# Performance work log

Measured on AMD Instinct MI355X. Metric: run time of the kernel, lower is better.

The kernel has to match this reference:

```python
import jax, jax.numpy as jnp
import numpy as np

N_NODES = 100000
N_EDGES = 1600000
F_IN, F_HID, F_OUT = 128, 256, 128


def setup_inputs() -> dict:
    key = jax.random.key(0)
    ks = jax.random.split(key, 9)
    x = jax.random.normal(ks[0], (N_NODES, F_IN), dtype=jnp.float32)
    edge_src = jax.random.randint(ks[1], (N_EDGES,), 0, N_NODES, dtype=jnp.int32)
    edge_dst = jax.random.randint(ks[2], (N_EDGES,), 0, N_NODES, dtype=jnp.int32)
    s1 = 1.0 / np.sqrt(F_IN)
    s2 = 1.0 / np.sqrt(F_HID)
    W_self1 = jax.random.uniform(ks[3], (F_IN, F_HID), jnp.float32, -s1, s1)
    W_neigh1 = jax.random.uniform(ks[4], (F_IN, F_HID), jnp.float32, -s1, s1)
    b1 = jnp.zeros((F_HID,), jnp.float32)
    W_self2 = jax.random.uniform(ks[5], (F_HID, F_OUT), jnp.float32, -s2, s2)
    W_neigh2 = jax.random.uniform(ks[6], (F_HID, F_OUT), jnp.float32, -s2, s2)
    b2 = jnp.zeros((F_OUT,), jnp.float32)
    return {"x": x, "edge_src": edge_src, "edge_dst": edge_dst,
            "W_self1": W_self1, "W_neigh1": W_neigh1, "b1": b1,
            "W_self2": W_self2, "W_neigh2": W_neigh2, "b2": b2}


def _sage_mean(h, src, dst, W_self, W_neigh, b):
    # mean-aggregate neighbor features onto dst nodes (DGL SAGEConv 'mean')
    deg = jax.ops.segment_sum(jnp.ones_like(src, dtype=h.dtype), dst,
                              num_segments=N_NODES)
    neigh_sum = jax.ops.segment_sum(h[src], dst, num_segments=N_NODES)
    neigh = neigh_sum / jnp.maximum(deg, 1.0)[:, None]
    return h @ W_self + neigh @ W_neigh + b


def reference(x, edge_src, edge_dst, W_self1, W_neigh1, b1, W_self2, W_neigh2, b2):
    h = _sage_mean(x, edge_src, edge_dst, W_self1, W_neigh1, b1)
    h = jax.nn.sigmoid(h)
    h = _sage_mean(h, edge_src, edge_dst, W_self2, W_neigh2, b2)
    return h
```

## Files before the change

### kernel.cpp

```cpp
#include <hip/hip_runtime.h>
#include <hip/hip_bf16.h>

#define N_NODES 100000
#define N_EDGES 1600000
#define F_IN 128
#define F_HID 256
#define F_OUT 128

typedef unsigned short ushort_t;
typedef __attribute__((ext_vector_type(4))) float f32x4;
typedef __attribute__((ext_vector_type(8))) short bf16x8;

#define GAS __attribute__((address_space(1)))
#define LAS __attribute__((address_space(3)))

__device__ __forceinline__ float bf2f(ushort_t u) {
    unsigned int x = ((unsigned int)u) << 16;
    return __builtin_bit_cast(float, x);
}
__device__ __forceinline__ ushort_t f2bf(float f) {
    unsigned int x = __builtin_bit_cast(unsigned int, f);
    unsigned int r = (x + 0x7fffu + ((x >> 16) & 1u)) >> 16;
    return (ushort_t)r;
}

#define NBUCK ((N_NODES + 255) >> 8)
#define CHUNK 4096

__global__ __launch_bounds__(256) void bucket_count_kernel(
    const int* __restrict__ dst, int* __restrict__ bucket_cnt, int n) {
    __shared__ int hist[NBUCK];
    int tid = threadIdx.x;
    int e0 = blockIdx.x * CHUNK;
    int cnt = n - e0; if (cnt > CHUNK) cnt = CHUNK;
    for (int b = tid; b < NBUCK; b += 256) hist[b] = 0;
    __syncthreads();
    for (int i = tid; i < cnt; i += 256) {
        int d = __builtin_nontemporal_load(dst + e0 + i);
        atomicAdd(&hist[d >> 8], 1);
    }
    __syncthreads();
    for (int b = tid; b < NBUCK; b += 256)
        if (hist[b]) atomicAdd(&bucket_cnt[b], hist[b]);
}

__global__ __launch_bounds__(512) void bucket_scan_kernel(
    const int* __restrict__ bucket_cnt, int* __restrict__ bbase,
    int* __restrict__ bcursor, int* __restrict__ rowptr) {
    __shared__ int tmp[512];
    int tid = threadIdx.x;
    int v = (tid < NBUCK) ? bucket_cnt[tid] : 0;
    tmp[tid] = v;
    __syncthreads();
#pragma unroll
    for (int off = 1; off < 512; off <<= 1) {
        int t = (tid >= off) ? tmp[tid - off] : 0;
        __syncthreads();
        tmp[tid] += t;
        __syncthreads();
    }
    if (tid < NBUCK) {
        int base = tmp[tid] - v;
        bbase[tid] = base;
        bcursor[tid] = base;
    }
    if (tid == 0) {
        bbase[NBUCK] = N_EDGES;
        rowptr[N_NODES] = N_EDGES;
    }
}

__global__ __launch_bounds__(256) void bin_edges_kernel(
    const int* __restrict__ src, const int* __restrict__ dst,
    int* __restrict__ bcursor, unsigned int* __restrict__ pairs, int n) {
    __shared__ int sdst[CHUNK];
    __shared__ int ssrc[CHUNK];
    __shared__ int hist[NBUCK];
    __shared__ int resv[NBUCK];
    int tid = threadIdx.x;
    int e0 = blockIdx.x * CHUNK;
    int cnt = n - e0; if (cnt > CHUNK) cnt = CHUNK;
    for (int b = tid; b < NBUCK; b += 256) hist[b] = 0;
    __syncthreads();
    for (int i = tid; i < cnt; i += 256) {
        int d = __builtin_nontemporal_load(dst + e0 + i);
        int s = __builtin_nontemporal_load(src + e0 + i);
        sdst[i] = d;
        ssrc[i] = s;
        atomicAdd(&hist[d >> 8], 1);
    }
    __syncthreads();
    for (int b = tid; b < NBUCK; b += 256) {
        int h = hist[b];
        resv[b] = h ? atomicAdd(&bcursor[b], h) : 0;
        hist[b] = 0;
    }
    __syncthreads();
    for (int i = tid; i < cnt; i += 256) {
        int d = sdst[i], s = ssrc[i];
        int b = d >> 8;
        int off = atomicAdd(&hist[b], 1);
        pairs[resv[b] + off] = ((unsigned)(d & 255) << 17) | (unsigned)s;
    }
}

__global__ __launch_bounds__(256) void sort_bucket_kernel(
    const unsigned int* __restrict__ pairs, const int* __restrict__ bbase,
    int* __restrict__ rowptr, float* __restrict__ invdeg,
    int* __restrict__ csr_src, int nNodes) {
    __shared__ int lcnt[256];
    __shared__ int lrp[256];
    int tid = threadIdx.x;
    int base = blockIdx.x << 8;
    int nn = nNodes - base; if (nn > 256) nn = 256;
    lcnt[tid] = 0;
    __syncthreads();
    int e0 = bbase[blockIdx.x], e1 = bbase[blockIdx.x + 1];
    for (int i = e0 + tid; i < e1; i += 256)
        atomicAdd(&lcnt[pairs[i] >> 17], 1);
    __syncthreads();
    int v = lcnt[tid];
    lrp[tid] = v;
    __syncthreads();
#pragma unroll
    for (int off = 1; off < 256; off <<= 1) {
        int t = (tid >= off) ? lrp[tid - off] : 0;
        __syncthreads();
        lrp[tid] += t;
        __syncthreads();
    }
    lcnt[tid] = 0;
    lrp[tid] = lrp[tid] - v + e0;
    if (tid < nn) {
        rowptr[base + tid] = lrp[tid];
        invdeg[base + tid] = 1.0f / fmaxf((float)v, 1.0f);
    }
    __syncthreads();
    for (int i = e0 + tid; i < e1; i += 256) {
        unsigned pv = pairs[i];
        int j = (int)(pv >> 17);
        int off = atomicAdd(&lcnt[j], 1);
        csr_src[lrp[j] + off] = (int)(pv & 0x1FFFFu);
    }
}

__global__ __launch_bounds__(256) void convert_x_kernel(const float* __restrict__ x,
                                                        ushort_t* __restrict__ xb, int n4) {
    int i = blockIdx.x * 256 + threadIdx.x;
    if (i >= n4) return;
    int e = i * 4;
    f32x4 v = __builtin_nontemporal_load((const f32x4*)(x + e));
    ushort4 o;
    o.x = f2bf(v.x); o.y = f2bf(v.y); o.z = f2bf(v.z); o.w = f2bf(v.w);
    *(ushort4*)(xb + e) = o;
}

__global__ __launch_bounds__(256) void wtransK_kernel(const float* __restrict__ W1,
                                                      const float* __restrict__ W2,
                                                      ushort_t* __restrict__ Wt,
                                                      int Kx, int Ktot, int N) {
    int i = blockIdx.x * 256 + threadIdx.x;
    if (i >= N * Ktot) return;
    int n = i / Ktot, k = i - n * Ktot;
    float v = (k < Kx) ? W1[(size_t)k * N + n] : W2[(size_t)(k - Kx) * N + n];
    Wt[(size_t)n * Ktot + k] = f2bf(v);
}

__global__ __launch_bounds__(256) void wtransN_kernel(const float* __restrict__ Wa,
                                                      const float* __restrict__ Wb,
                                                      ushort_t* __restrict__ Wt,
                                                      int K, int Nh) {
    int i = blockIdx.x * 256 + threadIdx.x;
    if (i >= 2 * Nh * K) return;
    int n = i / K, k = i - n * K;
    const float* W = (n < Nh) ? Wa : Wb;
    int nn = (n < Nh) ? n : n - Nh;
    Wt[(size_t)n * K + k] = f2bf(W[(size_t)k * Nh + nn]);
}

#define ACC8(arr, v)                                                \
    arr[0] += bf2f((ushort_t)((v).x & 0xffffu));                    \
    arr[1] += bf2f((ushort_t)((v).x >> 16));                        \
    arr[2] += bf2f((ushort_t)((v).y & 0xffffu));                    \
    arr[3] += bf2f((ushort_t)((v).y >> 16));                        \
    arr[4] += bf2f((ushort_t)((v).z & 0xffffu));                    \
    arr[5] += bf2f((ushort_t)((v).z >> 16));                        \
    arr[6] += bf2f((ushort_t)((v).w & 0xffffu));                    \
    arr[7] += bf2f((ushort_t)((v).w >> 16));

template <int MODE>
__global__ __launch_bounds__(256) void gather2_kernel(
    const ushort_t* __restrict__ H,
    const int* __restrict__ rowptr,
    const int* __restrict__ csr_src,
    const float* __restrict__ invdeg,
    const ushort_t* __restrict__ uself,
    const float* __restrict__ bias,
    void* __restrict__ outp,
    int nNodes, int totWaves) {
    int lane = threadIdx.x & 63;
    int wv = blockIdx.x * 4 + (threadIdx.x >> 6);
    int grp = lane >> 4, sub = lane & 15;
    const size_t cofs = (size_t)sub * 8;
    int pair = wv;
    if (pair * 2 >= nNodes) return;
    int r0 = rowptr[pair * 2];
    int r1 = rowptr[pair * 2 + 1];
    int r2 = rowptr[pair * 2 + 2];
    while (true) {
        int npair = pair + totWaves;
        bool hasNext = (npair * 2 < nNodes);
        int n0 = 0, n1 = 0, n2 = 0;
        if (hasNext) {
            n0 = rowptr[npair * 2];
            n1 = rowptr[npair * 2 + 1];
            n2 = rowptr[npair * 2 + 2];
        }
        int nodeA = pair * 2;
        int sA = r0, eA = r1, sB = r1, eB = r2;
        int cA = sA < N_EDGES ? sA : N_EDGES - 1;
        int cB = sB < N_EDGES ? sB : N_EDGES - 1;
        float accA[8] = {}, accB[8] = {};
        for (int ea = sA + grp, eb = sB + grp; ea < eA || eb < eB; ea += 16, eb += 16) {
            bool pa0 = ea < eA, pa1 = ea + 4 < eA, pa2 = ea + 8 < eA, pa3 = ea + 12 < eA;
            bool pb0 = eb < eB, pb1 = eb + 4 < eB, pb2 = eb + 8 < eB, pb3 = eb + 12 < eB;
            int ja0 = pa0 ? ea : cA, ja1 = pa1 ? ea + 4 : cA;
            int ja2 = pa2 ? ea + 8 : cA, ja3 = pa3 ? ea + 12 : cA;
            int jb0 = pb0 ? eb : cB, jb1 = pb1 ? eb + 4 : cB;
            int jb2 = pb2 ? eb + 8 : cB, jb3 = pb3 ? eb + 12 : cB;
            int sa0 = csr_src[ja0], sa1 = csr_src[ja1];
            int sa2 = csr_src[ja2], sa3 = csr_src[ja3];
            int sb0 = csr_src[jb0], sb1 = csr_src[jb1];
            int sb2 = csr_src[jb2], sb3 = csr_src[jb3];
            uint4 va0 = *(const uint4*)(H + (size_t)sa0 * 128 + cofs);
            uint4 va1 = *(const uint4*)(H + (size_t)sa1 * 128 + cofs);
            uint4 va2 = *(const uint4*)(H + (size_t)sa2 * 128 + cofs);
            uint4 va3 = *(const uint4*)(H + (size_t)sa3 * 128 + cofs);
            uint4 vb0 = *(const uint4*)(H + (size_t)sb0 * 128 + cofs);
            uint4 vb1 = *(const uint4*)(H + (size_t)sb1 * 128 + cofs);
            uint4 vb2 = *(const uint4*)(H + (size_t)sb2 * 128 + cofs);
            uint4 vb3 = *(const uint4*)(H + (size_t)sb3 * 128 + cofs);
            if (pa0) { ACC8(accA, va0); }
            if (pa1) { ACC8(accA, va1); }
            if (pa2) { ACC8(accA, va2); }
            if (pa3) { ACC8(accA, va3); }
            if (pb0) { ACC8(accB, vb0); }
            if (pb1) { ACC8(accB, vb1); }
            if (pb2) { ACC8(accB, vb2); }
            if (pb3) { ACC8(accB, vb3); }
        }
#pragma unroll
        for (int j = 0; j < 8; ++j) {
            accA[j] += __shfl_xor(accA[j], 16);
            accA[j] += __shfl_xor(accA[j], 32);
            accB[j] += __shfl_xor(accB[j], 16);
            accB[j] += __shfl_xor(accB[j], 32);
        }
        if (grp == 0) {
            int nodeB = nodeA + 1;
            float scA = invdeg[nodeA];
            float scB = (nodeB < nNodes) ? invdeg[nodeB] : 1.0f;
            if (MODE == 0) {
                uint4 o;
                o.x = (unsigned)f2bf(accA[0] * scA) | ((unsigned)f2bf(accA[1] * scA) << 16);
                o.y = (unsigned)f2bf(accA[2] * scA) | ((unsigned)f2bf(accA[3] * scA) << 16);
                o.z = (unsigned)f2bf(accA[4] * scA) | ((unsigned)f2bf(accA[5] * scA) << 16);
                o.w = (unsigned)f2bf(accA[6] * scA) | ((unsigned)f2bf(accA[7] * scA) << 16);
                *(uint4*)((ushort_t*)outp + (size_t)nodeA * 128 + cofs) = o;
                if (nodeB < nNodes) {
                    uint4 p2;
                    p2.x = (unsigned)f2bf(accB[0] * scB) | ((unsigned)f2bf(accB[1] * scB) << 16);
                    p2.y = (unsigned)f2bf(accB[2] * scB) | ((unsigned)f2bf(accB[3] * scB) << 16);
                    p2.z = (unsigned)f2bf(accB[4] * scB) | ((unsigned)f2bf(accB[5] * scB) << 16);
                    p2.w = (unsigned)f2bf(accB[6] * scB) | ((unsigned)f2bf(accB[7] * scB) << 16);
                    *(uint4*)((ushort_t*)outp + (size_t)nodeB * 128 + cofs) = p2;
                }
            } else {
                uint4 us = *(const uint4*)(uself + (size_t)nodeA * 128 + cofs);
                f32x4 o0, o1;
                o0.x = accA[0] * scA + bf2f((ushort_t)(us.x & 0xffffu)) + bias[cofs + 0];
                o0.y = accA[1] * scA + bf2f((ushort_t)(us.x >> 16)) + bias[cofs + 1];
                o0.z = accA[2] * scA + bf2f((ushort_t)(us.y & 0xffffu)) + bias[cofs + 2];
                o0.w = accA[3] * scA + bf2f((ushort_t)(us.y >> 16)) + bias[cofs + 3];
                o1.x = accA[4] * scA + bf2f((ushort_t)(us.z & 0xffffu)) + bias[cofs + 4];
                o1.y = accA[5] * scA + bf2f((ushort_t)(us.z >> 16)) + bias[cofs + 5];
                o1.z = accA[6] * scA + bf2f((ushort_t)(us.w & 0xffffu)) + bias[cofs + 6];
                o1.w = accA[7] * scA + bf2f((ushort_t)(us.w >> 16)) + bias[cofs + 7];
                float* op = (float*)outp + (size_t)nodeA * 128 + cofs;
                __builtin_nontemporal_store(o0, (f32x4*)op);
                __builtin_nontemporal_store(o1, (f32x4*)(op + 4));
                if (nodeB < nNodes) {
                    uint4 u2 = *(const uint4*)(uself + (size_t)nodeB * 128 + cofs);
                    f32x4 q0, q1;
                    q0.x = accB[0] * scB + bf2f((ushort_t)(u2.x & 0xffffu)) + bias[cofs + 0];
                    q0.y = accB[1] * scB + bf2f((ushort_t)(u2.x >> 16)) + bias[cofs + 1];
                    q0.z = accB[2] * scB + bf2f((ushort_t)(u2.y & 0xffffu)) + bias[cofs + 2];
                    q0.w = accB[3] * scB + bf2f((ushort_t)(u2.y >> 16)) + bias[cofs + 3];
                    q1.x = accB[4] * scB + bf2f((ushort_t)(u2.z & 0xffffu)) + bias[cofs + 4];
                    q1.y = accB[5] * scB + bf2f((ushort_t)(u2.z >> 16)) + bias[cofs + 5];
                    q1.z = accB[6] * scB + bf2f((ushort_t)(u2.w & 0xffffu)) + bias[cofs + 6];
                    q1.w = accB[7] * scB + bf2f((ushort_t)(u2.w >> 16)) + bias[cofs + 7];
                    float* oq = (float*)outp + (size_t)nodeB * 128 + cofs;
                    __builtin_nontemporal_store(q0, (f32x4*)oq);
                    __builtin_nontemporal_store(q1, (f32x4*)(oq + 4));
                }
            }
        }
        if (!hasNext) break;
        pair = npair; r0 = n0; r1 = n1; r2 = n2;
    }
}

__global__ __launch_bounds__(512) void gemm_fused_kernel(
    const ushort_t* __restrict__ xb,
    const ushort_t* __restrict__ agg,
    const ushort_t* __restrict__ Wt1,
    const float* __restrict__ b1,
    const ushort_t* __restrict__ Wt2,
    ushort_t* __restrict__ uself,
    ushort_t* __restrict__ uneigh,
    int M) {
    __shared__ ushort_t hs[64 * 256];
    __shared__ ushort_t Asb[2][64 * 32];
    __shared__ ushort_t Bsb[2][256 * 32];
    int tid = threadIdx.x;
    int lane = tid & 63, wid = tid >> 6;
    int l15 = lane & 15, kgrp = lane >> 4;
    int bm = blockIdx.x * 64;
    int wr = (wid >> 2) * 32, wc = (wid & 3) * 64;

    auto stageA = [&](int buf, int t) {
        if (wid >= 4) return;
        int k0 = t * 32;
        const ushort_t* Ap = (k0 < 128) ? xb : agg;
        int kk0 = k0 & 127;
        int row = wid * 16 + (lane >> 2);
        int scol = ((lane & 3) ^ (row & 3)) << 3;
        int ar = bm + row; if (ar > M - 1) ar = M - 1;
        __builtin_amdgcn_global_load_lds(
            (const GAS void*)(Ap + (size_t)ar * 128 + kk0 + scol),
            (LAS void*)(&Asb[buf][wid * 512]), 16, 0, 0);
    };
    auto stageB = [&](int buf, int t, const ushort_t* Bt) {
        int k0 = t * 32;
#pragma unroll
        for (int t2 = 0; t2 < 2; ++t2) {
            int c = wid * 2 + t2;
            int row = c * 16 + (lane >> 2);
            int scol = ((lane & 3) ^ (row & 3)) << 3;
            __builtin_amdgcn_global_load_lds(
                (const GAS void*)(Bt + (size_t)row * 256 + k0 + scol),
                (LAS void*)(&Bsb[buf][c * 512]), 16, 0, 0);
        }
    };

    f32x4 acc[2][4] = {};

    stageA(0, 0); stageB(0, 0, Wt1);
    __syncthreads();
#pragma unroll
    for (int t = 0; t < 8; ++t) {
        int buf = t & 1;
        if (t < 7) { stageA(buf ^ 1, t + 1); stageB(buf ^ 1, t + 1, Wt1); }
        bf16x8 af[2], bfv[4];
#pragma unroll
        for (int mi = 0; mi < 2; ++mi) {
            int row = wr + mi * 16 + l15;
            af[mi] = *(const bf16x8*)(&Asb[buf][row * 32 + ((kgrp ^ (row & 3)) << 3)]);
        }
#pragma unroll
        for (int ni = 0; ni < 4; ++ni) {
            int row = wc + ni * 16 + l15;
            bfv[ni] = *(const bf16x8*)(&Bsb[buf][row * 32 + ((kgrp ^ (row & 3)) << 3)]);
        }
#pragma unroll
        for (int mi = 0; mi < 2; ++mi)
#pragma unroll
            for (int ni = 0; ni < 4; ++ni)
                acc[mi][ni] = __builtin_amdgcn_mfma_f32_16x16x32_bf16(
                    af[mi], bfv[ni], acc[mi][ni], 0, 0, 0);
        __syncthreads();
    }

#pragma unroll
    for (int mi = 0; mi < 2; ++mi) {
#pragma unroll
        for (int ni = 0; ni < 4; ++ni) {
            int hcol = wc + ni * 16 + l15;
            float bv = b1[hcol];
#pragma unroll
            for (int r = 0; r < 4; ++r) {
                float v = acc[mi][ni][r] + bv;
                v = 1.0f / (1.0f + __expf(-v));
                int lr = wr + mi * 16 + kgrp * 4 + r;
                hs[lr * 256 + (hcol ^ ((lr & 7) << 3))] = f2bf(v);
                acc[mi][ni][r] = 0.0f;
            }
        }
    }
    stageB(0, 0, Wt2);
    __syncthreads();
#pragma unroll
    for (int t = 0; t < 8; ++t) {
        int buf = t & 1;
        if (t < 7) stageB(buf ^ 1, t + 1, Wt2);
        int k0 = t * 32;
        bf16x8 af[2], bfv[4];
#pragma unroll
        for (int mi = 0; mi < 2; ++mi) {
            int row = wr + mi * 16 + l15;
            int c = k0 + kgrp * 8;
            af[mi] = *(const bf16x8*)(&hs[row * 256 + (c ^ ((row & 7) << 3))]);
        }
#pragma unroll
        for (int ni = 0; ni < 4; ++ni) {
            int row = wc + ni * 16 + l15;
            bfv[ni] = *(const bf16x8*)(&Bsb[buf][row * 32 + ((kgrp ^ (row & 3)) << 3)]);
        }
#pragma unroll
        for (int mi = 0; mi < 2; ++mi)
#pragma unroll
            for (int ni = 0; ni < 4; ++ni)
                acc[mi][ni] = __builtin_amdgcn_mfma_f32_16x16x32_bf16(
                    af[mi], bfv[ni], acc[mi][ni], 0, 0, 0);
        __syncthreads();
    }

    ushort_t* my = hs + wid * 1024;
#pragma unroll
    for (int mi = 0; mi < 2; ++mi) {
#pragma unroll
        for (int ni = 0; ni < 4; ++ni) {
#pragma unroll
            for (int r = 0; r < 4; ++r) {
                int lr = kgrp * 4 + r;
                int lc = (ni * 16 + l15) ^ (kgrp << 3);
                my[lr * 64 + lc] = f2bf(acc[mi][ni][r]);
            }
        }
#pragma unroll
        for (int it = 0; it < 2; ++it) {
            int r2 = (lane >> 3) + it * 8;
            int swz = ((r2 >> 2) & 3) << 3;
            int c2 = ((lane & 7) << 3) ^ swz;
            bf16x8 vv = *(const bf16x8*)(&my[r2 * 64 + c2]);
            int grow = bm + wr + mi * 16 + r2;
            if (grow < M) {
                int gc = wc + (c2 ^ swz);
                ushort_t* dstp = (gc < 128)
                    ? uself + (size_t)grow * 128 + gc
                    : uneigh + (size_t)grow * 128 + (gc - 128);
                *(bf16x8*)dstp = vv;
            }
        }
    }
}

extern "C" void kernel_launch(void* const* d_in, const int* in_sizes, int n_in,
                              void* d_out, int out_size, void* d_ws, size_t ws_size,
                              hipStream_t stream) {
    const float* x        = (const float*)d_in[0];
    const int*   src      = (const int*)d_in[1];
    const int*   dst      = (const int*)d_in[2];
    const float* W_self1  = (const float*)d_in[3];
    const float* W_neigh1 = (const float*)d_in[4];
    const float* b1       = (const float*)d_in[5];
    const float* W_self2  = (const float*)d_in[6];
    const float* W_neigh2 = (const float*)d_in[7];
    const float* b2       = (const float*)d_in[8];
    float* out = (float*)d_out;

    char* p = (char*)d_ws;
    auto alloc = [&](size_t bytes) { char* r = p; p += (bytes + 255) & ~(size_t)255; return r; };
    float*    invdeg   = (float*)alloc((size_t)N_NODES * 4);
    ushort_t* xb       = (ushort_t*)alloc((size_t)N_NODES * 128 * 2);
    ushort_t* agg      = (ushort_t*)alloc((size_t)N_NODES * 128 * 2);
    ushort_t* uself    = (ushort_t*)alloc((size_t)N_NODES * 128 * 2);
    ushort_t* uneigh   = (ushort_t*)alloc((size_t)N_NODES * 128 * 2);
    ushort_t* Wt1      = (ushort_t*)alloc((size_t)256 * 256 * 2);
    ushort_t* Wt2      = (ushort_t*)alloc((size_t)256 * 256 * 2);
    int* rowptr        = (int*)alloc((size_t)(N_NODES + 1) * 4);
    int* bucket_cnt    = (int*)alloc((size_t)NBUCK * 4);
    int* bbase         = (int*)alloc((size_t)(NBUCK + 1) * 4);
    int* bcursor       = (int*)alloc((size_t)NBUCK * 4);
    unsigned int* pairs= (unsigned int*)alloc((size_t)N_EDGES * 4);
    int* csr_src       = (int*)alloc((size_t)N_EDGES * 4);

    convert_x_kernel<<<(N_NODES * F_IN / 4 + 255) / 256, 256, 0, stream>>>(
        x, xb, N_NODES * F_IN / 4);
    wtransK_kernel<<<(256 * 256 + 255) / 256, 256, 0, stream>>>(
        W_self1, W_neigh1, Wt1, 128, 256, 256);
    wtransN_kernel<<<(256 * 256 + 255) / 256, 256, 0, stream>>>(
        W_self2, W_neigh2, Wt2, 256, 128);

    hipMemsetAsync(bucket_cnt, 0, (size_t)NBUCK * sizeof(int), stream);
    bucket_count_kernel<<<(N_EDGES + CHUNK - 1) / CHUNK, 256, 0, stream>>>(
        dst, bucket_cnt, N_EDGES);
    bucket_scan_kernel<<<1, 512, 0, stream>>>(bucket_cnt, bbase, bcursor, rowptr);
    bin_edges_kernel<<<(N_EDGES + CHUNK - 1) / CHUNK, 256, 0, stream>>>(
        src, dst, bcursor, pairs, N_EDGES);
    sort_bucket_kernel<<<NBUCK, 256, 0, stream>>>(
        pairs, bbase, rowptr, invdeg, csr_src, N_NODES);

    const int GATHER_BLOCKS = 2048;
    const int TOT_WAVES = GATHER_BLOCKS * 4;

    gather2_kernel<0><<<GATHER_BLOCKS, 256, 0, stream>>>(
        xb, rowptr, csr_src, invdeg, nullptr, nullptr, agg, N_NODES, TOT_WAVES);
    {
        dim3 grid((N_NODES + 63) / 64);
        gemm_fused_kernel<<<grid, 512, 0, stream>>>(
            xb, agg, Wt1, b1, Wt2, uself, uneigh, N_NODES);
    }
    gather2_kernel<1><<<GATHER_BLOCKS, 256, 0, stream>>>(
        uneigh, rowptr, csr_src, invdeg, uself, b2, out, N_NODES, TOT_WAVES);
}
```

Baseline: 273.5 us.

## Replace count/scan binning with fixed-capacity buckets and fuse weight transposes

Drops the bucket-count and bucket-scan kernels by giving each destination bucket a fixed capacity region (BCAP slots), so bin_edges can scatter directly using per-bucket cursors. Row boundaries become start/end int2 pairs per node, since the CSR is no longer contiguous. The two weight-transpose kernels are merged into one launch. This removes launches and a full pass over dst, but relies on no bucket exceeding 8192 edges and enlarges the pairs and csr_src buffers.

```diff
diff --git a/kernel.cpp b/kernel.cpp
--- a/kernel.cpp
+++ b/kernel.cpp
@@ -26,49 +26,7 @@
 
 #define NBUCK ((N_NODES + 255) >> 8)
 #define CHUNK 4096
-
-__global__ __launch_bounds__(256) void bucket_count_kernel(
-    const int* __restrict__ dst, int* __restrict__ bucket_cnt, int n) {
-    __shared__ int hist[NBUCK];
-    int tid = threadIdx.x;
-    int e0 = blockIdx.x * CHUNK;
-    int cnt = n - e0; if (cnt > CHUNK) cnt = CHUNK;
-    for (int b = tid; b < NBUCK; b += 256) hist[b] = 0;
-    __syncthreads();
-    for (int i = tid; i < cnt; i += 256) {
-        int d = __builtin_nontemporal_load(dst + e0 + i);
-        atomicAdd(&hist[d >> 8], 1);
-    }
-    __syncthreads();
-    for (int b = tid; b < NBUCK; b += 256)
-        if (hist[b]) atomicAdd(&bucket_cnt[b], hist[b]);
-}
-
-__global__ __launch_bounds__(512) void bucket_scan_kernel(
-    const int* __restrict__ bucket_cnt, int* __restrict__ bbase,
-    int* __restrict__ bcursor, int* __restrict__ rowptr) {
-    __shared__ int tmp[512];
-    int tid = threadIdx.x;
-    int v = (tid < NBUCK) ? bucket_cnt[tid] : 0;
-    tmp[tid] = v;
-    __syncthreads();
-#pragma unroll
-    for (int off = 1; off < 512; off <<= 1) {
-        int t = (tid >= off) ? tmp[tid - off] : 0;
-        __syncthreads();
-        tmp[tid] += t;
-        __syncthreads();
-    }
-    if (tid < NBUCK) {
-        int base = tmp[tid] - v;
-        bbase[tid] = base;
-        bcursor[tid] = base;
-    }
-    if (tid == 0) {
-        bbase[NBUCK] = N_EDGES;
-        rowptr[N_NODES] = N_EDGES;
-    }
-}
+#define BCAP 8192
 
 __global__ __launch_bounds__(256) void bin_edges_kernel(
     const int* __restrict__ src, const int* __restrict__ dst,
@@ -92,7 +50,7 @@
     __syncthreads();
     for (int b = tid; b < NBUCK; b += 256) {
         int h = hist[b];
-        resv[b] = h ? atomicAdd(&bcursor[b], h) : 0;
+        resv[b] = h ? (b * BCAP + atomicAdd(&bcursor[b], h)) : 0;
         hist[b] = 0;
     }
     __syncthreads();
@@ -105,8 +63,8 @@
 }
 
 __global__ __launch_bounds__(256) void sort_bucket_kernel(
-    const unsigned int* __restrict__ pairs, const int* __restrict__ bbase,
-    int* __restrict__ rowptr, float* __restrict__ invdeg,
+    const unsigned int* __restrict__ pairs, const int* __restrict__ bcursor,
+    int2* __restrict__ rowse, float* __restrict__ invdeg,
     int* __restrict__ csr_src, int nNodes) {
     __shared__ int lcnt[256];
     __shared__ int lrp[256];
@@ -115,7 +73,8 @@
     int nn = nNodes - base; if (nn > 256) nn = 256;
     lcnt[tid] = 0;
     __syncthreads();
-    int e0 = bbase[blockIdx.x], e1 = bbase[blockIdx.x + 1];
+    int e0 = blockIdx.x * BCAP;
+    int e1 = e0 + bcursor[blockIdx.x];
     for (int i = e0 + tid; i < e1; i += 256)
         atomicAdd(&lcnt[pairs[i] >> 17], 1);
     __syncthreads();
@@ -132,7 +91,7 @@
     lcnt[tid] = 0;
     lrp[tid] = lrp[tid] - v + e0;
     if (tid < nn) {
-        rowptr[base + tid] = lrp[tid];
+        rowse[base + tid] = make_int2(lrp[tid], lrp[tid] + v);
         invdeg[base + tid] = 1.0f / fmaxf((float)v, 1.0f);
     }
     __syncthreads();
@@ -155,27 +114,22 @@
     *(ushort4*)(xb + e) = o;
 }
 
-__global__ __launch_bounds__(256) void wtransK_kernel(const float* __restrict__ W1,
-                                                      const float* __restrict__ W2,
-                                                      ushort_t* __restrict__ Wt,
-                                                      int Kx, int Ktot, int N) {
+__global__ __launch_bounds__(256) void wtrans_both_kernel(
+    const float* __restrict__ Ws1, const float* __restrict__ Wn1,
+    const float* __restrict__ Ws2, const float* __restrict__ Wn2,
+    ushort_t* __restrict__ Wt1, ushort_t* __restrict__ Wt2) {
     int i = blockIdx.x * 256 + threadIdx.x;
-    if (i >= N * Ktot) return;
-    int n = i / Ktot, k = i - n * Ktot;
-    float v = (k < Kx) ? W1[(size_t)k * N + n] : W2[(size_t)(k - Kx) * N + n];
-    Wt[(size_t)n * Ktot + k] = f2bf(v);
-}
-
-__global__ __launch_bounds__(256) void wtransN_kernel(const float* __restrict__ Wa,
-                                                      const float* __restrict__ Wb,
-                                                      ushort_t* __restrict__ Wt,
-                                                      int K, int Nh) {
-    int i = blockIdx.x * 256 + threadIdx.x;
-    if (i >= 2 * Nh * K) return;
-    int n = i / K, k = i - n * K;
-    const float* W = (n < Nh) ? Wa : Wb;
-    int nn = (n < Nh) ? n : n - Nh;
-    Wt[(size_t)n * K + k] = f2bf(W[(size_t)k * Nh + nn]);
+    if (i < 65536) {
+        int n = i >> 8, k = i & 255;
+        float v = (k < 128) ? Ws1[(size_t)k * 256 + n] : Wn1[(size_t)(k - 128) * 256 + n];
+        Wt1[(size_t)n * 256 + k] = f2bf(v);
+    } else {
+        int j = i - 65536;
+        int n = j >> 8, k = j & 255;
+        const float* W = (n < 128) ? Ws2 : Wn2;
+        int nn = (n < 128) ? n : n - 128;
+        Wt2[(size_t)n * 256 + k] = f2bf(W[(size_t)k * 128 + nn]);
+    }
 }
 
 #define ACC8(arr, v)                                                \
@@ -191,7 +145,7 @@
 template <int MODE>
 __global__ __launch_bounds__(256) void gather2_kernel(
     const ushort_t* __restrict__ H,
-    const int* __restrict__ rowptr,
+    const int2* __restrict__ rowse,
     const int* __restrict__ csr_src,
     const float* __restrict__ invdeg,
     const ushort_t* __restrict__ uself,
@@ -204,22 +158,19 @@
     const size_t cofs = (size_t)sub * 8;
     int pair = wv;
     if (pair * 2 >= nNodes) return;
-    int r0 = rowptr[pair * 2];
-    int r1 = rowptr[pair * 2 + 1];
-    int r2 = rowptr[pair * 2 + 2];
+    int2 ra = rowse[pair * 2];
+    int2 rb = rowse[pair * 2 + 1];
     while (true) {
         int npair = pair + totWaves;
         bool hasNext = (npair * 2 < nNodes);
-        int n0 = 0, n1 = 0, n2 = 0;
+        int2 na = make_int2(0, 0), nb = make_int2(0, 0);
         if (hasNext) {
-            n0 = rowptr[npair * 2];
-            n1 = rowptr[npair * 2 + 1];
-            n2 = rowptr[npair * 2 + 2];
+            na = rowse[npair * 2];
+            nb = rowse[npair * 2 + 1];
         }
         int nodeA = pair * 2;
-        int sA = r0, eA = r1, sB = r1, eB = r2;
-        int cA = sA < N_EDGES ? sA : N_EDGES - 1;
-        int cB = sB < N_EDGES ? sB : N_EDGES - 1;
+        int sA = ra.x, eA = ra.y, sB = rb.x, eB = rb.y;
+        int cA = sA, cB = sB;
         float accA[8] = {}, accB[8] = {};
         for (int ea = sA + grp, eb = sB + grp; ea < eA || eb < eB; ea += 16, eb += 16) {
             bool pa0 = ea < eA, pa1 = ea + 4 < eA, pa2 = ea + 8 < eA, pa3 = ea + 12 < eA;
@@ -259,7 +210,7 @@
         if (grp == 0) {
             int nodeB = nodeA + 1;
             float scA = invdeg[nodeA];
-            float scB = (nodeB < nNodes) ? invdeg[nodeB] : 1.0f;
+            float scB = invdeg[nodeB];
             if (MODE == 0) {
                 uint4 o;
                 o.x = (unsigned)f2bf(accA[0] * scA) | ((unsigned)f2bf(accA[1] * scA) << 16);
@@ -267,14 +218,12 @@
                 o.z = (unsigned)f2bf(accA[4] * scA) | ((unsigned)f2bf(accA[5] * scA) << 16);
                 o.w = (unsigned)f2bf(accA[6] * scA) | ((unsigned)f2bf(accA[7] * scA) << 16);
                 *(uint4*)((ushort_t*)outp + (size_t)nodeA * 128 + cofs) = o;
-                if (nodeB < nNodes) {
-                    uint4 p2;
-                    p2.x = (unsigned)f2bf(accB[0] * scB) | ((unsigned)f2bf(accB[1] * scB) << 16);
-                    p2.y = (unsigned)f2bf(accB[2] * scB) | ((unsigned)f2bf(accB[3] * scB) << 16);
-                    p2.z = (unsigned)f2bf(accB[4] * scB) | ((unsigned)f2bf(accB[5] * scB) << 16);
-                    p2.w = (unsigned)f2bf(accB[6] * scB) | ((unsigned)f2bf(accB[7] * scB) << 16);
-                    *(uint4*)((ushort_t*)outp + (size_t)nodeB * 128 + cofs) = p2;
-                }
+                uint4 p2;
+                p2.x = (unsigned)f2bf(accB[0] * scB) | ((unsigned)f2bf(accB[1] * scB) << 16);
+                p2.y = (unsigned)f2bf(accB[2] * scB) | ((unsigned)f2bf(accB[3] * scB) << 16);
+                p2.z = (unsigned)f2bf(accB[4] * scB) | ((unsigned)f2bf(accB[5] * scB) << 16);
+                p2.w = (unsigned)f2bf(accB[6] * scB) | ((unsigned)f2bf(accB[7] * scB) << 16);
+                *(uint4*)((ushort_t*)outp + (size_t)nodeB * 128 + cofs) = p2;
             } else {
                 uint4 us = *(const uint4*)(uself + (size_t)nodeA * 128 + cofs);
                 f32x4 o0, o1;
@@ -289,25 +238,23 @@
                 float* op = (float*)outp + (size_t)nodeA * 128 + cofs;
                 __builtin_nontemporal_store(o0, (f32x4*)op);
                 __builtin_nontemporal_store(o1, (f32x4*)(op + 4));
-                if (nodeB < nNodes) {
-                    uint4 u2 = *(const uint4*)(uself + (size_t)nodeB * 128 + cofs);
-                    f32x4 q0, q1;
-                    q0.x = accB[0] * scB + bf2f((ushort_t)(u2.x & 0xffffu)) + bias[cofs + 0];
-                    q0.y = accB[1] * scB + bf2f((ushort_t)(u2.x >> 16)) + bias[cofs + 1];
-                    q0.z = accB[2] * scB + bf2f((ushort_t)(u2.y & 0xffffu)) + bias[cofs + 2];
-                    q0.w = accB[3] * scB + bf2f((ushort_t)(u2.y >> 16)) + bias[cofs + 3];
-                    q1.x = accB[4] * scB + bf2f((ushort_t)(u2.z & 0xffffu)) + bias[cofs + 4];
-                    q1.y = accB[5] * scB + bf2f((ushort_t)(u2.z >> 16)) + bias[cofs + 5];
-                    q1.z = accB[6] * scB + bf2f((ushort_t)(u2.w & 0xffffu)) + bias[cofs + 6];
-                    q1.w = accB[7] * scB + bf2f((ushort_t)(u2.w >> 16)) + bias[cofs + 7];
-                    float* oq = (float*)outp + (size_t)nodeB * 128 + cofs;
-                    __builtin_nontemporal_store(q0, (f32x4*)oq);
-                    __builtin_nontemporal_store(q1, (f32x4*)(oq + 4));
-                }
+                uint4 u2 = *(const uint4*)(uself + (size_t)nodeB * 128 + cofs);
+                f32x4 q0, q1;
+                q0.x = accB[0] * scB + bf2f((ushort_t)(u2.x & 0xffffu)) + bias[cofs + 0];
+                q0.y = accB[1] * scB + bf2f((ushort_t)(u2.x >> 16)) + bias[cofs + 1];
+                q0.z = accB[2] * scB + bf2f((ushort_t)(u2.y & 0xffffu)) + bias[cofs + 2];
+                q0.w = accB[3] * scB + bf2f((ushort_t)(u2.y >> 16)) + bias[cofs + 3];
+                q1.x = accB[4] * scB + bf2f((ushort_t)(u2.z & 0xffffu)) + bias[cofs + 4];
+                q1.y = accB[5] * scB + bf2f((ushort_t)(u2.z >> 16)) + bias[cofs + 5];
+                q1.z = accB[6] * scB + bf2f((ushort_t)(u2.w & 0xffffu)) + bias[cofs + 6];
+                q1.w = accB[7] * scB + bf2f((ushort_t)(u2.w >> 16)) + bias[cofs + 7];
+                float* oq = (float*)outp + (size_t)nodeB * 128 + cofs;
+                __builtin_nontemporal_store(q0, (f32x4*)oq);
+                __builtin_nontemporal_store(q1, (f32x4*)(oq + 4));
             }
         }
         if (!hasNext) break;
-        pair = npair; r0 = n0; r1 = n1; r2 = n2;
+        pair = npair; ra = na; rb = nb;
     }
 }
 
@@ -479,39 +426,32 @@
     ushort_t* uneigh   = (ushort_t*)alloc((size_t)N_NODES * 128 * 2);
     ushort_t* Wt1      = (ushort_t*)alloc((size_t)256 * 256 * 2);
     ushort_t* Wt2      = (ushort_t*)alloc((size_t)256 * 256 * 2);
-    int* rowptr        = (int*)alloc((size_t)(N_NODES + 1) * 4);
-    int* bucket_cnt    = (int*)alloc((size_t)NBUCK * 4);
-    int* bbase         = (int*)alloc((size_t)(NBUCK + 1) * 4);
+    int2* rowse        = (int2*)alloc((size_t)N_NODES * 8);
     int* bcursor       = (int*)alloc((size_t)NBUCK * 4);
-    unsigned int* pairs= (unsigned int*)alloc((size_t)N_EDGES * 4);
-    int* csr_src       = (int*)alloc((size_t)N_EDGES * 4);
+    unsigned int* pairs= (unsigned int*)alloc((size_t)NBUCK * BCAP * 4);
+    int* csr_src       = (int*)alloc((size_t)NBUCK * BCAP * 4);
 
     convert_x_kernel<<<(N_NODES * F_IN / 4 + 255) / 256, 256, 0, stream>>>(
         x, xb, N_NODES * F_IN / 4);
-    wtransK_kernel<<<(256 * 256 + 255) / 256, 256, 0, stream>>>(
-        W_self1, W_neigh1, Wt1, 128, 256, 256);
-    wtransN_kernel<<<(256 * 256 + 255) / 256, 256, 0, stream>>>(
-        W_self2, W_neigh2, Wt2, 256, 128);
-
-    hipMemsetAsync(bucket_cnt, 0, (size_t)NBUCK * sizeof(int), stream);
-    bucket_count_kernel<<<(N_EDGES + CHUNK - 1) / CHUNK, 256, 0, stream>>>(
-        dst, bucket_cnt, N_EDGES);
-    bucket_scan_kernel<<<1, 512, 0, stream>>>(bucket_cnt, bbase, bcursor, rowptr);
+    wtrans_both_kernel<<<(2 * 65536) / 256, 256, 0, stream>>>(
+        W_self1, W_neigh1, W_self2, W_neigh2, Wt1, Wt2);
+
+    hipMemsetAsync(bcursor, 0, (size_t)NBUCK * sizeof(int), stream);
     bin_edges_kernel<<<(N_EDGES + CHUNK - 1) / CHUNK, 256, 0, stream>>>(
         src, dst, bcursor, pairs, N_EDGES);
     sort_bucket_kernel<<<NBUCK, 256, 0, stream>>>(
-        pairs, bbase, rowptr, invdeg, csr_src, N_NODES);
+        pairs, bcursor, rowse, invdeg, csr_src, N_NODES);
 
     const int GATHER_BLOCKS = 2048;
     const int TOT_WAVES = GATHER_BLOCKS * 4;
 
     gather2_kernel<0><<<GATHER_BLOCKS, 256, 0, stream>>>(
-        xb, rowptr, csr_src, invdeg, nullptr, nullptr, agg, N_NODES, TOT_WAVES);
+        xb, rowse, csr_src, invdeg, nullptr, nullptr, agg, N_NODES, TOT_WAVES);
     {
         dim3 grid((N_NODES + 63) / 64);
         gemm_fused_kernel<<<grid, 512, 0, stream>>>(
             xb, agg, Wt1, b1, Wt2, uself, uneigh, N_NODES);
     }
     gather2_kernel<1><<<GATHER_BLOCKS, 256, 0, stream>>>(
-        uneigh, rowptr, csr_src, invdeg, uself, b2, out, N_NODES, TOT_WAVES);
-}
+        uneigh, rowse, csr_src, invdeg, uself, b2, out, N_NODES, TOT_WAVES);
+}
```

Measured after the change: 255.1 us. 6.7% less time.
